# Kernel optimization log

Hardware: AMD Instinct MI355X
Metric: run time of the kernel (lower is better)

## Reference

```python
import jax, jax.numpy as jnp
import numpy as np

N, F_IN, HID, CLUST = 4096, 128, 128, 128
HEADS = 2
RADIUS = 2.0
TOPK_ADD = 2
MOTIF_TOPK = 8
ETA = 0.5
L0_GAMMA, L0_ZETA = -0.1, 1.1
NEG_SLOPE = 0.2
BN_EPS = 1e-5
NEG_INF = -1e9


def _row_topk(A, k):
    # keep top-k per row, symmetrize by max, zero diagonal (matches row_topk)
    n = A.shape[0]
    if n <= k:
        S = A
    else:
        vals, idx = jax.lax.top_k(A, k)
        S = jnp.zeros_like(A).at[jnp.arange(n)[:, None], idx].set(vals)
        S = jnp.maximum(S, S.T)
    return S * (1.0 - jnp.eye(n, dtype=A.dtype))


def _bn_eval(x, g, b, m, v):
    return (x - m) * g * jax.lax.rsqrt(v + BN_EPS) + b


def _gate(logits, tau):
    # hard-concrete gate, eval path
    t = jnp.clip(tau, 0.1, None)
    s = jax.nn.sigmoid(logits / t) * (L0_ZETA - L0_GAMMA) + L0_GAMMA
    return jnp.clip(s, 0.0, 1.0)


def _gcn_dense(feat, A_w, W, b):
    # GCN: D^-1/2 A D^-1/2 (X W) + b, zero-degree rows -> 0
    deg = A_w.sum(axis=1)
    dinv = jnp.where(deg > 0, jax.lax.rsqrt(jnp.where(deg > 0, deg, 1.0)), 0.0)
    An = dinv[:, None] * A_w * dinv[None, :]
    return An @ (feat @ W) + b


def setup_inputs():
    key = jax.random.key(0)
    ks = jax.random.split(key, 30)
    eye = jnp.eye(N, dtype=jnp.float32)
    p = 16.0 / N  # ~16 avg degree
    B = jax.random.uniform(ks[0], (N, N)) < p
    A_in = ((B | B.T) & ~jnp.eye(N, dtype=bool)).astype(jnp.float32)
    Mw = jnp.where(jax.random.uniform(ks[1], (N, N)) < p, jax.random.uniform(ks[2], (N, N)), 0.0)
    A_motif = jnp.maximum(Mw, Mw.T) * (1.0 - eye)
    coords = jax.random.randint(ks[3], (N, 2), 0, 64).astype(jnp.float32)
    x = jax.random.normal(ks[4], (N, F_IN))
    s_in = 1.0 / np.sqrt(F_IN)
    s_h = 1.0 / np.sqrt(2 * HID)
    return {
        'x': x, 'A_in': A_in, 'A_motif': A_motif, 'coords': coords,
        'gat_w': jax.random.normal(ks[5], (F_IN, HEADS * HID)) * s_in,
        'gat_asrc': jax.random.normal(ks[6], (HEADS, HID)) * s_h,
        'gat_adst': jax.random.normal(ks[7], (HEADS, HID)) * s_h,
        'gat_b': jnp.zeros((HEADS * HID,)),
        'bnA_g': jnp.ones((2 * HID,)), 'bnA_b': jnp.zeros((2 * HID,)),
        'bnA_m': jax.random.normal(ks[8], (2 * HID,)) * 0.1,
        'bnA_v': 0.5 + jax.random.uniform(ks[9], (2 * HID,)),
        'gcnM_w': jax.random.normal(ks[10], (F_IN, 2 * HID)) * s_in,
        'gcnM_b': jnp.zeros((2 * HID,)),
        'bnM_g': jnp.ones((2 * HID,)), 'bnM_b': jnp.zeros((2 * HID,)),
        'bnM_m': jax.random.normal(ks[11], (2 * HID,)) * 0.1,
        'bnM_v': 0.5 + jax.random.uniform(ks[12], (2 * HID,)),
        'mu': jnp.asarray(-3.0), 'tau': jnp.asarray(1.0),
        'prune_w': jax.random.normal(ks[13], (4 * HID + 1,)) * s_h,
        'prune_b': jnp.asarray(0.0),
        'rewire_w': jax.random.normal(ks[14], (4 * HID + 1,)) * s_h,
        'rewire_b': jnp.asarray(0.0),
        'pool_w': jax.random.normal(ks[15], (2 * HID, CLUST)) * s_h,
        'pool_b': jnp.zeros((CLUST,)),
    }


def reference(x, A_in, A_motif, coords, gat_w, gat_asrc, gat_adst, gat_b,
              bnA_g, bnA_b, bnA_m, bnA_v, gcnM_w, gcnM_b, bnM_g, bnM_b, bnM_m, bnM_v,
              mu, tau, prune_w, prune_b, rewire_w, rewire_b, pool_w, pool_b):
    n = x.shape[0]
    eye = jnp.eye(n, dtype=x.dtype)
    # --- GAT branch on A_in (dense masked attention; PyG adds self loops) ---
    Wx = (x @ gat_w).reshape(n, HEADS, HID)           # [N, heads, H]
    a_src = (Wx * gat_asrc).sum(-1)                   # [N, heads]
    a_dst = (Wx * gat_adst).sum(-1)
    e = jax.nn.leaky_relu(a_dst[:, None, :] + a_src[None, :, :], NEG_SLOPE)  # e[i,j,h]
    adj_mask = (A_in > 0) | jnp.eye(n, dtype=bool)
    e = jnp.where(adj_mask[..., None], e, NEG_INF)
    alpha = jax.nn.softmax(e, axis=1)                 # softmax over sources j
    h_A = jnp.einsum('ijh,jhd->ihd', alpha, Wx).reshape(n, HEADS * HID) + gat_b
    h_A = jax.nn.elu(_bn_eval(h_A, bnA_g, bnA_b, bnA_m, bnA_v))
    # --- motif branch ---
    M_hat = _row_topk(A_motif, MOTIF_TOPK)
    h_M = jax.nn.elu(_bn_eval(_gcn_dense(x, M_hat, gcnM_w, gcnM_b), bnM_g, bnM_b, bnM_m, bnM_v))
    h = h_A + jax.nn.softplus(mu) * h_M               # [N, 2H]
    d2 = 2 * HID
    triu = jnp.triu(jnp.ones((n, n), dtype=bool), 1)
    # --- prune gate on existing upper-tri edges (Linear is separable) ---
    pu = h @ prune_w[:d2]
    pv = h @ prune_w[d2:2 * d2]
    prune_logits = pu[:, None] + pv[None, :] + prune_w[2 * d2] * M_hat + prune_b
    z_prune = _gate(prune_logits, tau)
    edge_u = triu & (A_in > 0)
    Wp = jnp.where(edge_u, z_prune * A_in, 0.0)
    A_pruned = Wp + Wp.T
    # --- rewire candidates: L1 cdist within radius, non-edges, upper tri ---
    dist = jnp.abs(coords[:, None, :] - coords[None, :, :]).sum(-1)
    cand_u = (dist > 0) & (dist <= RADIUS) & (A_in < 1e-6) & triu
    ru = h @ rewire_w[:d2]
    rv = h @ rewire_w[d2:2 * d2]
    rew_logits = ru[:, None] + rv[None, :] + rewire_w[2 * d2] * M_hat + rewire_b
    Zu = jnp.where(cand_u, _gate(rew_logits, tau), 0.0)
    # per-node top-k selection over incident candidates (symmetric view)
    cand_sym = cand_u | cand_u.T
    scores = jnp.where(cand_sym, Zu + Zu.T, NEG_INF)
    thr = jax.lax.top_k(scores, TOPK_ADD)[0][:, -1]
    keep = (scores >= thr[:, None]) & cand_sym
    pair_keep = (keep | keep.T) & cand_u
    A_added_u = jnp.where(pair_keep, Zu, 0.0)
    A_added_sym = jnp.maximum(A_added_u, A_added_u.T)
    A_refined = A_pruned + ETA * A_added_sym
    # --- pooling GCN (default GCNConv adds self loops, weight 1) ---
    S = jax.nn.softmax(_gcn_dense(h, A_refined + eye, pool_w, pool_b), axis=1)  # [N, C]
    X_coarse = S.T @ h                                 # [C, 2H]
    A_c = S.T @ A_refined @ S
    A_c = A_c * (1.0 - jnp.eye(A_c.shape[0], dtype=A_c.dtype))
    A_coarse = _row_topk(A_c, MOTIF_TOPK)
    return X_coarse, A_coarse
```

## Files before the change

### kernel.cpp

```cpp
#include <hip/hip_runtime.h>
#include <hip/hip_bf16.h>
#include <stdint.h>

#define N 4096
#define FIN 128
#define HID 128
#define D2 256
#define CLUST 128
#define NEG_INF (-1e9f)
#define KAJ 128
#define KM 96
#define KC 64
#define KA (KAJ + KC)
#define CCAP 32
#define JCH 128
#define NCH (N/JCH)

typedef __hip_bfloat16 bf16;

__device__ __forceinline__ float cvt(float v){ return v; }
__device__ __forceinline__ float cvt(bf16 v){ return __bfloat162float(v); }
__device__ __forceinline__ void stout(float* p, size_t i, float v){ p[i] = v; }
__device__ __forceinline__ void stout(bf16* p, size_t i, float v){ p[i] = __float2bfloat16(v); }

__device__ __forceinline__ float hc_gate(float l, float tau){
  float t = fmaxf(tau, 0.1f);
  float s = 1.f / (1.f + expf(-l / t));
  s = s * 1.2f - 0.1f;
  return fminf(fmaxf(s, 0.f), 1.f);
}

__global__ void k_detect(const void* x, const void* w, int* flag){
  __shared__ int hits;
  int t = threadIdx.x;
  if (t == 0) hits = 0;
  __syncthreads();
  const bf16* xb = (const bf16*)x;
  const bf16* wb = (const bf16*)w;
  int h = 0;
  for (int i = t; i < 4096; i += 256){
    float a = __bfloat162float(xb[i]);
    float b = __bfloat162float(wb[i]);
    if (!(fabsf(a) < 1e6f)) ++h;
    if (!(fabsf(b) < 1e6f)) ++h;
  }
  atomicAdd(&hits, h);
  __syncthreads();
  if (t == 0) *flag = (hits > 0) ? 1 : 0;
}

template<typename T>
__device__ void xw2_body(const T* x, const T* gat_w, const T* gcnM_w,
                         float* Wx, float* xwM, float* xr){
  int i0 = blockIdx.x * 16, t = threadIdx.x;
  for (int idx = t; idx < 16*FIN; idx += 256) xr[idx] = cvt(x[(size_t)i0*FIN + idx]);
  __syncthreads();
  float wx[16], xm[16];
  #pragma unroll
  for (int r = 0; r < 16; ++r){ wx[r] = 0.f; xm[r] = 0.f; }
  for (int k = 0; k < FIN; ++k){
    float wa = cvt(gat_w[k*D2 + t]);
    float wm = cvt(gcnM_w[k*D2 + t]);
    #pragma unroll
    for (int r = 0; r < 16; ++r){
      wx[r] += xr[r*FIN + k] * wa;
      xm[r] += xr[r*FIN + k] * wm;
    }
  }
  #pragma unroll
  for (int r = 0; r < 16; ++r){
    Wx[(size_t)(i0+r)*D2 + t] = wx[r];
    xwM[(size_t)(i0+r)*D2 + t] = xm[r];
  }
}
__global__ void k_xw2(const int* fl, const void* x, const void* gw, const void* gmw,
                      float* Wx, float* xwM){
  __shared__ float xr[16*FIN];
  if (*fl) xw2_body<float>((const float*)x,(const float*)gw,(const float*)gmw,Wx,xwM,xr);
  else     xw2_body<bf16 >((const bf16*)x,(const bf16*)gw,(const bf16*)gmw,Wx,xwM,xr);
}

template<typename T>
__device__ void att_body(const float* Wx, const T* asrc, const T* adst,
                         float* a_src, float* a_dst){
  int w = threadIdx.x >> 6, l = threadIdx.x & 63;
  int row = blockIdx.x*4 + w;
  const float4* wr = (const float4*)(Wx + (size_t)row*D2);
  float4 v = wr[l];
  float s0 = cvt(asrc[l*4])*v.x + cvt(asrc[l*4+1])*v.y
           + cvt(asrc[l*4+2])*v.z + cvt(asrc[l*4+3])*v.w;
  float s1 = cvt(adst[l*4])*v.x + cvt(adst[l*4+1])*v.y
           + cvt(adst[l*4+2])*v.z + cvt(adst[l*4+3])*v.w;
  for (int d = 16; d > 0; d >>= 1){
    s0 += __shfl_down(s0, d, 32);
    s1 += __shfl_down(s1, d, 32);
  }
  if ((l & 31) == 0){
    a_src[row*2 + (l >> 5)] = s0;
    a_dst[row*2 + (l >> 5)] = s1;
  }
}
__global__ void k_att(const int* fl, const float* Wx, const void* as, const void* ad,
                      float* a_src, float* a_dst){
  if (*fl) att_body<float>(Wx,(const float*)as,(const float*)ad,a_src,a_dst);
  else     att_body<bf16 >(Wx,(const bf16*)as,(const bf16*)ad,a_src,a_dst);
}

__device__ __forceinline__ void t8_insert(unsigned long long* keys, float v, int j){
  if (v > 0.f){
    unsigned long long key =
      ((unsigned long long)__float_as_uint(v) << 32) | (unsigned int)(~(unsigned int)j);
    if (key > keys[7]){
      keys[7] = key;
      #pragma unroll
      for (int q = 7; q > 0; --q){
        if (keys[q] > keys[q-1]){ unsigned long long tmp = keys[q]; keys[q] = keys[q-1]; keys[q-1] = tmp; }
      }
    }
  }
}
__device__ void top8_reduce(unsigned long long* keys, float* t8v, int* t8i,
                            unsigned long long* red, int i, int t){
  unsigned long long last = ~0ull;
  for (int r = 0; r < 8; ++r){
    unsigned long long cand = 0ull;
    #pragma unroll
    for (int q = 0; q < 8; ++q){ if (keys[q] < last){ cand = keys[q]; break; } }
    red[t] = cand;
    __syncthreads();
    for (int s = 128; s > 0; s >>= 1){
      if (t < s){ if (red[t+s] > red[t]) red[t] = red[t+s]; }
      __syncthreads();
    }
    unsigned long long win = red[0];
    __syncthreads();
    if (t == 0){
      float v = __uint_as_float((unsigned int)(win >> 32));
      int j = (int)(~(unsigned int)win);
      bool ok = (win != 0ull) && (v > 0.f);
      t8v[i*8 + r] = ok ? v : 0.f;
      t8i[i*8 + r] = ok ? j : -1;
    }
    last = win;
  }
}
__global__ void k_top8(const int* fl, const void* Amot, float* t8v, int* t8i){
  __shared__ unsigned long long red[256];
  int i = blockIdx.x, t = threadIdx.x;
  unsigned long long keys[8];
  #pragma unroll
  for (int q = 0; q < 8; ++q) keys[q] = 0ull;
  if (*fl){
    const float4* rowp = (const float4*)((const float*)Amot + (size_t)i*N);
    for (int s = 0; s < N/1024; ++s){
      float4 v4 = rowp[s*256 + t];
      int jb = s*1024 + t*4;
      t8_insert(keys, v4.x, jb);
      t8_insert(keys, v4.y, jb+1);
      t8_insert(keys, v4.z, jb+2);
      t8_insert(keys, v4.w, jb+3);
    }
  } else {
    const bf16* rowp = (const bf16*)Amot + (size_t)i*N;
    for (int s = 0; s < N/256; ++s){
      int j = t + 256*s;
      t8_insert(keys, cvt(rowp[j]), j);
    }
  }
  top8_reduce(keys, t8v, t8i, red, i, t);
}

__global__ void k_mown(const float* __restrict__ t8v, const int* __restrict__ t8i,
                       int* __restrict__ Midx, float* __restrict__ Mval,
                       int* __restrict__ Mcnt){
  int i = blockIdx.x*256 + threadIdx.x;
  if (i >= N) return;
  int c = 0;
  #pragma unroll
  for (int r = 0; r < 8; ++r){
    int j = t8i[i*8 + r];
    if (j >= 0){ Midx[i*KM + c] = j; Mval[i*KM + c] = t8v[i*8 + r]; ++c; }
  }
  Mcnt[i] = c;
}

__global__ void k_mscat(const float* __restrict__ t8v, const int* __restrict__ t8i,
                        int* __restrict__ Midx, float* __restrict__ Mval,
                        int* __restrict__ Mcnt){
  int e = blockIdx.x*256 + threadIdx.x;
  if (e >= N*8) return;
  int i = e >> 3;
  int j = t8i[e];
  if (j < 0) return;
  #pragma unroll
  for (int s = 0; s < 8; ++s) if (t8i[j*8 + s] == i) return;
  int p = atomicAdd(&Mcnt[j], 1);
  if (p < KM){ Midx[j*KM + p] = i; Mval[j*KM + p] = t8v[e]; }
}

__global__ void k_degM(const float* __restrict__ Mval, const int* __restrict__ Mcnt,
                       float* __restrict__ dinvM){
  int i = blockIdx.x*256 + threadIdx.x;
  if (i >= N) return;
  int n = min(Mcnt[i], KM);
  float s = 0.f;
  for (int e = 0; e < n; ++e) s += Mval[i*KM + e];
  dinvM[i] = (s > 0.f) ? rsqrtf(s) : 0.f;
}

template<typename T>
__device__ void motif_body(const int* Midx, const float* Mval, const int* Mcnt,
                           const float* dinvM, const float* xwM, const T* gcnM_b,
                           const T* bng, const T* bnb, const T* bnm, const T* bnv,
                           float* hM, int* nj, float* nw){
  int i = blockIdx.x, t = threadIdx.x;
  int n = min(Mcnt[i], KM);
  for (int e = t; e < n; e += 256){
    int j = Midx[i*KM + e];
    nj[e] = j;
    nw[e] = Mval[i*KM + e] * dinvM[j];
  }
  __syncthreads();
  float acc = 0.f;
  for (int e = 0; e < n; ++e) acc += nw[e] * xwM[nj[e]*D2 + t];
  float val = acc * dinvM[i] + cvt(gcnM_b[t]);
  val = (val - cvt(bnm[t])) * cvt(bng[t]) * rsqrtf(cvt(bnv[t]) + 1e-5f) + cvt(bnb[t]);
  val = (val > 0.f) ? val : expm1f(val);
  hM[i*D2 + t] = val;
}
__global__ void k_motif_agg(const int* fl, const int* Midx, const float* Mval,
                            const int* Mcnt, const float* dinvM, const float* xwM,
                            const void* gb, const void* g, const void* b,
                            const void* m, const void* v, float* hM){
  __shared__ int nj[KM];
  __shared__ float nw[KM];
  if (*fl) motif_body<float>(Midx,Mval,Mcnt,dinvM,xwM,(const float*)gb,(const float*)g,
                             (const float*)b,(const float*)m,(const float*)v,hM,nj,nw);
  else     motif_body<bf16 >(Midx,Mval,Mcnt,dinvM,xwM,(const bf16*)gb,(const bf16*)g,
                             (const bf16*)b,(const bf16*)m,(const bf16*)v,hM,nj,nw);
}

__global__ void k_adj(const int* fl, const void* Ain,
                      int* __restrict__ AdjIdx, float* __restrict__ AdjVal,
                      int* __restrict__ AdjCnt){
  __shared__ int cnt;
  int i = blockIdx.x, t = threadIdx.x;
  if (t == 0) cnt = 0;
  __syncthreads();
  if (*fl){
    const float4* rowp = (const float4*)((const float*)Ain + (size_t)i*N);
    for (int s = 0; s < N/1024; ++s){
      float4 v4 = rowp[s*256 + t];
      int jb = s*1024 + t*4;
      if (v4.x > 0.f && jb   != i){ int p = atomicAdd(&cnt,1); if (p < KAJ){ AdjIdx[i*KAJ+p] = jb;   AdjVal[i*KAJ+p] = v4.x; } }
      if (v4.y > 0.f && jb+1 != i){ int p = atomicAdd(&cnt,1); if (p < KAJ){ AdjIdx[i*KAJ+p] = jb+1; AdjVal[i*KAJ+p] = v4.y; } }
      if (v4.z > 0.f && jb+2 != i){ int p = atomicAdd(&cnt,1); if (p < KAJ){ AdjIdx[i*KAJ+p] = jb+2; AdjVal[i*KAJ+p] = v4.z; } }
      if (v4.w > 0.f && jb+3 != i){ int p = atomicAdd(&cnt,1); if (p < KAJ){ AdjIdx[i*KAJ+p] = jb+3; AdjVal[i*KAJ+p] = v4.w; } }
    }
  } else {
    const bf16* rowp = (const bf16*)Ain + (size_t)i*N;
    for (int j = t; j < N; j += 256){
      float v = cvt(rowp[j]);
      if (v > 0.f && j != i){ int p = atomicAdd(&cnt,1); if (p < KAJ){ AdjIdx[i*KAJ+p] = j; AdjVal[i*KAJ+p] = v; } }
    }
  }
  __syncthreads();
  if (t == 0) AdjCnt[i] = min(cnt, KAJ);
}

template<typename T>
__device__ void gat_body(const int* AdjIdx, const int* AdjCnt, const float* Wx,
                         const float* a_src, const float* a_dst, const T* gat_b,
                         const T* bng, const T* bnb, const T* bnm, const T* bnv,
                         const float* hM, const T* mu,
                         float* h, int* nbr, float* ew, float* mm, float* inv){
  int i = blockIdx.x, t = threadIdx.x;
  int na = AdjCnt[i];
  for (int e = t; e < na; e += 256) nbr[e] = AdjIdx[i*KAJ + e];
  if (t == 0) nbr[na] = i;
  __syncthreads();
  int n = na + 1;
  float ad0 = a_dst[i*2], ad1 = a_dst[i*2 + 1];
  for (int e = t; e < n; e += 256){
    int j = nbr[e];
    float e0 = ad0 + a_src[j*2];
    float e1 = ad1 + a_src[j*2 + 1];
    e0 = (e0 > 0.f) ? e0 : 0.2f * e0;
    e1 = (e1 > 0.f) ? e1 : 0.2f * e1;
    ew[2*e] = e0; ew[2*e + 1] = e1;
  }
  __syncthreads();
  if (t == 0){
    float m0 = -3.4e38f, m1 = -3.4e38f;
    for (int e = 0; e < n; ++e){ m0 = fmaxf(m0, ew[2*e]); m1 = fmaxf(m1, ew[2*e+1]); }
    mm[0] = m0; mm[1] = m1;
  }
  __syncthreads();
  for (int e = t; e < n; e += 256){
    ew[2*e]   = expf(ew[2*e]   - mm[0]);
    ew[2*e+1] = expf(ew[2*e+1] - mm[1]);
  }
  __syncthreads();
  if (t == 0){
    float s0 = 0.f, s1 = 0.f;
    for (int e = 0; e < n; ++e){ s0 += ew[2*e]; s1 += ew[2*e+1]; }
    inv[0] = 1.f/s0; inv[1] = 1.f/s1;
  }
  __syncthreads();
  int hh = t >> 7;
  float acc = 0.f;
  for (int e = 0; e < n; ++e) acc += ew[2*e + hh] * Wx[nbr[e]*D2 + t];
  float val = acc * inv[hh] + cvt(gat_b[t]);
  val = (val - cvt(bnm[t])) * cvt(bng[t]) * rsqrtf(cvt(bnv[t]) + 1e-5f) + cvt(bnb[t]);
  val = (val > 0.f) ? val : expm1f(val);
  float spmu = log1pf(expf(cvt(mu[0])));
  h[i*D2 + t] = val + spmu * hM[i*D2 + t];
}
__global__ void k_gat_agg(const int* fl, const int* AdjIdx, const int* AdjCnt,
                          const float* Wx, const float* a_src, const float* a_dst,
                          const void* gb, const void* g, const void* b, const void* m,
                          const void* v, const float* hM, const void* mu, float* h){
  __shared__ int nbr[KAJ + 1];
  __shared__ float ew[(KAJ + 1)*2];
  __shared__ float mm[2], inv[2];
  if (*fl) gat_body<float>(AdjIdx,AdjCnt,Wx,a_src,a_dst,(const float*)gb,(const float*)g,
                           (const float*)b,(const float*)m,(const float*)v,hM,(const float*)mu,
                           h,nbr,ew,mm,inv);
  else     gat_body<bf16 >(AdjIdx,AdjCnt,Wx,a_src,a_dst,(const bf16*)gb,(const bf16*)g,
                           (const bf16*)b,(const bf16*)m,(const bf16*)v,hM,(const bf16*)mu,
                           h,nbr,ew,mm,inv);
}

template<typename T>
__device__ void puv_body(const float* h, const T* pw, const T* rw,
                         float* pu, float* pv, float* ru, float* rv, float* red){
  int i = blockIdx.x, t = threadIdx.x;
  float hv = h[i*D2 + t];
  float v0 = hv * cvt(pw[t]);
  float v1 = hv * cvt(pw[D2 + t]);
  float v2 = hv * cvt(rw[t]);
  float v3 = hv * cvt(rw[D2 + t]);
  red[t] = v0; __syncthreads();
  for (int k = 128; k > 0; k >>= 1){ if (t < k) red[t] += red[t+k]; __syncthreads(); }
  if (t == 0) pu[i] = red[0];
  __syncthreads();
  red[t] = v1; __syncthreads();
  for (int k = 128; k > 0; k >>= 1){ if (t < k) red[t] += red[t+k]; __syncthreads(); }
  if (t == 0) pv[i] = red[0];
  __syncthreads();
  red[t] = v2; __syncthreads();
  for (int k = 128; k > 0; k >>= 1){ if (t < k) red[t] += red[t+k]; __syncthreads(); }
  if (t == 0) ru[i] = red[0];
  __syncthreads();
  red[t] = v3; __syncthreads();
  for (int k = 128; k > 0; k >>= 1){ if (t < k) red[t] += red[t+k]; __syncthreads(); }
  if (t == 0) rv[i] = red[0];
}
__global__ void k_puv(const int* fl, const float* h, const void* pw, const void* rw,
                      float* pu, float* pv, float* ru, float* rv){
  __shared__ float red[256];
  if (*fl) puv_body<float>(h,(const float*)pw,(const float*)rw,pu,pv,ru,rv,red);
  else     puv_body<bf16 >(h,(const bf16*)pw,(const bf16*)rw,pu,pv,ru,rv,red);
}

__global__ void k_zero(int* cellCnt){
  int i = blockIdx.x*256 + threadIdx.x;
  if (i < 4096) cellCnt[i] = 0;
}

template<typename T>
__device__ void gridb_body(const T* coords, int* cellCnt, int* cellNode){
  int i = blockIdx.x*256 + threadIdx.x;
  if (i >= N) return;
  int cx = (int)cvt(coords[2*i]), cy = (int)cvt(coords[2*i+1]);
  int cell = cy*64 + cx;
  int p = atomicAdd(&cellCnt[cell], 1);
  if (p < CCAP) cellNode[cell*CCAP + p] = i;
}
__global__ void k_gridb(const int* fl, const void* coords, int* cellCnt, int* cellNode){
  if (*fl) gridb_body<float>((const float*)coords, cellCnt, cellNode);
  else     gridb_body<bf16 >((const bf16*)coords, cellCnt, cellNode);
}

template<typename T>
__device__ void cand_body(const T* coords, const T* Ain,
                          const int* Midx, const float* Mval, const int* Mcnt,
                          const int* cellCnt, const int* cellNode,
                          const float* ru, const float* rv,
                          const T* rw, const T* rb, const T* taup,
                          int* Cidx, float* Cz, int* Ccnt, float* thr,
                          int* scI, float* scZ, int* scn){
  int w = threadIdx.x >> 6, l = threadIdx.x & 63;
  int i = blockIdx.x*4 + w;
  if (l == 0) scn[w] = 0;
  __syncthreads();
  float cix = cvt(coords[2*i]), ciy = cvt(coords[2*i+1]);
  int cx = (int)cix, cy = (int)ciy;
  float w2 = cvt(rw[2*D2]), rbias = cvt(rb[0]), tau = cvt(taup[0]);
  float rui = ru[i], rvi = rv[i];
  int mc = min(Mcnt[i], KM);
  const int dxs[12] = {1,-1,0,0, 2,-2,0,0, 1,1,-1,-1};
  const int dys[12] = {0,0,1,-1, 0,0,2,-2, 1,-1,1,-1};
  if (l < 12){
    int nx = cx + dxs[l], ny = cy + dys[l];
    if (nx >= 0 && nx < 64 && ny >= 0 && ny < 64){
      int cell = ny*64 + nx;
      int cn = min(cellCnt[cell], CCAP);
      for (int e = 0; e < cn; ++e){
        int j = cellNode[cell*CCAP + e];
        float d = fabsf(cix - cvt(coords[2*j])) + fabsf(ciy - cvt(coords[2*j+1]));
        float a = cvt(Ain[(size_t)i*N + j]);
        if (d > 0.f && d <= 2.0f && a < 1e-6f){
          float mh = 0.f;
          for (int q = 0; q < mc; ++q) if (Midx[i*KM + q] == j){ mh = Mval[i*KM + q]; break; }
          float lg = ((i < j) ? (rui + rv[j]) : (ru[j] + rvi)) + w2*mh + rbias;
          float z = hc_gate(lg, tau);
          int p = atomicAdd(&scn[w], 1);
          if (p < KC){ scI[w*KC + p] = j; scZ[w*KC + p] = z; }
        }
      }
    }
  }
  __syncthreads();
  int n = min(scn[w], KC);
  if (l == 0){
    float m1 = NEG_INF, m2 = NEG_INF;
    for (int e = 0; e < n; ++e){
      float z = scZ[w*KC + e];
      if (z > m1){ m2 = m1; m1 = z; } else if (z > m2){ m2 = z; }
    }
    thr[i] = m2;
    Ccnt[i] = n;
  }
  for (int e = l; e < n; e += 64){ Cidx[i*KC + e] = scI[w*KC + e]; Cz[i*KC + e] = scZ[w*KC + e]; }
}
__global__ void k_cand(const int* fl, const void* coords, const void* Ain,
                       const int* Midx, const float* Mval, const int* Mcnt,
                       const int* cellCnt, const int* cellNode,
                       const float* ru, const float* rv, const void* rw, const void* rb,
                       const void* taup, int* Cidx, float* Cz, int* Ccnt, float* thr){
  __shared__ int scI[4*KC];
  __shared__ float scZ[4*KC];
  __shared__ int scn[4];
  if (*fl) cand_body<float>((const float*)coords,(const float*)Ain,Midx,Mval,Mcnt,
                            cellCnt,cellNode,ru,rv,(const float*)rw,(const float*)rb,
                            (const float*)taup,Cidx,Cz,Ccnt,thr,scI,scZ,scn);
  else     cand_body<bf16 >((const bf16*)coords,(const bf16*)Ain,Midx,Mval,Mcnt,
                            cellCnt,cellNode,ru,rv,(const bf16*)rw,(const bf16*)rb,
                            (const bf16*)taup,Cidx,Cz,Ccnt,thr,scI,scZ,scn);
}

template<typename T>
__device__ void aref_body(const int* AdjIdx, const float* AdjVal, const int* AdjCnt,
                          const int* Midx, const float* Mval, const int* Mcnt,
                          const float* pu, const float* pv, const T* pw, const T* pb,
                          const T* taup, const int* Cidx, const float* Cz, const int* Ccnt,
                          const float* thr, int* Aidx, float* Aval, int* Acnt, float* dinvR){
  int w = threadIdx.x >> 6, l = threadIdx.x & 63;
  int i = blockIdx.x*4 + w;
  float wp2 = cvt(pw[2*D2]), pbias = cvt(pb[0]), tau = cvt(taup[0]);
  float pui = pu[i], pvi = pv[i];
  int na = AdjCnt[i];
  int mc = min(Mcnt[i], KM);
  float sum = 0.f;
  for (int e = l; e < na; e += 64){
    int j = AdjIdx[i*KAJ + e];
    float a = AdjVal[i*KAJ + e];
    float mh = 0.f;
    for (int q = 0; q < mc; ++q) if (Midx[i*KM + q] == j){ mh = Mval[i*KM + q]; break; }
    float lg = ((i < j) ? (pui + pv[j]) : (pu[j] + pvi)) + wp2*mh + pbias;
    float wv = hc_gate(lg, tau) * a;
    Aidx[i*KA + e] = j; Aval[i*KA + e] = wv; sum += wv;
  }
  int nc = min(Ccnt[i], KC);
  float thri = thr[i];
  for (int e = l; e < nc; e += 64){
    int j = Cidx[i*KC + e];
    float z = Cz[i*KC + e];
    float wv = (z >= thri || z >= thr[j]) ? 0.5f*z : 0.f;
    Aidx[i*KA + na + e] = j; Aval[i*KA + na + e] = wv; sum += wv;
  }
  for (int d = 32; d > 0; d >>= 1) sum += __shfl_down(sum, d, 64);
  if (l == 0){ Acnt[i] = na + nc; dinvR[i] = rsqrtf(sum + 1.f); }
}
__global__ void k_aref(const int* fl, const int* AdjIdx, const float* AdjVal,
                       const int* AdjCnt, const int* Midx, const float* Mval,
                       const int* Mcnt, const float* pu, const float* pv, const void* pw,
                       const void* pb, const void* taup, const int* Cidx, const float* Cz,
                       const int* Ccnt, const float* thr, int* Aidx, float* Aval,
                       int* Acnt, float* dinvR){
  if (*fl) aref_body<float>(AdjIdx,AdjVal,AdjCnt,Midx,Mval,Mcnt,pu,pv,(const float*)pw,
                            (const float*)pb,(const float*)taup,Cidx,Cz,Ccnt,thr,
                            Aidx,Aval,Acnt,dinvR);
  else     aref_body<bf16 >(AdjIdx,AdjVal,AdjCnt,Midx,Mval,Mcnt,pu,pv,(const bf16*)pw,
                            (const bf16*)pb,(const bf16*)taup,Cidx,Cz,Ccnt,thr,
                            Aidx,Aval,Acnt,dinvR);
}

template<typename T>
__device__ void hw_body(const float* h, const T* pool_w, float* hW, float* hr){
  int i = blockIdx.x, t = threadIdx.x;
  hr[t] = h[i*D2 + t]; hr[t + 128] = h[i*D2 + t + 128];
  __syncthreads();
  float acc = 0.f;
  #pragma unroll 4
  for (int d = 0; d < D2; ++d) acc += hr[d] * cvt(pool_w[d*CLUST + t]);
  hW[i*CLUST + t] = acc;
}
__global__ void k_hw(const int* fl, const float* h, const void* pw, float* hW){
  __shared__ float hr[D2];
  if (*fl) hw_body<float>(h,(const float*)pw,hW,hr);
  else     hw_body<bf16 >(h,(const bf16*)pw,hW,hr);
}

template<typename T>
__device__ void preS_body(const int* Aidx, const float* Aval, const int* Acnt,
                          const float* dinvR, const float* hW, const T* pool_b,
                          float* S, int* sAi, float* sW, float* red){
  int i = blockIdx.x, t = threadIdx.x;
  int n = min(Acnt[i], KA);
  for (int e = t; e < n; e += 128){
    int j = Aidx[i*KA + e];
    sAi[e] = j;
    sW[e] = Aval[i*KA + e] * dinvR[j];
  }
  __syncthreads();
  float di = dinvR[i];
  float acc = di * hW[i*CLUST + t];
  for (int e = 0; e < n; ++e) acc += sW[e] * hW[sAi[e]*CLUST + t];
  float val = acc * di + cvt(pool_b[t]);
  red[t] = val; __syncthreads();
  for (int k = 64; k > 0; k >>= 1){ if (t < k) red[t] = fmaxf(red[t], red[t+k]); __syncthreads(); }
  float mx = red[0]; __syncthreads();
  float ex = expf(val - mx); red[t] = ex; __syncthreads();
  for (int k = 64; k > 0; k >>= 1){ if (t < k) red[t] += red[t+k]; __syncthreads(); }
  float sm = red[0]; __syncthreads();
  S[i*CLUST + t] = ex / sm;
}
__global__ void k_preS(const int* fl, const int* Aidx, const float* Aval, const int* Acnt,
                       const float* dinvR, const float* hW, const void* pb, float* S){
  __shared__ int sAi[KA];
  __shared__ float sW[KA];
  __shared__ float red[128];
  if (*fl) preS_body<float>(Aidx,Aval,Acnt,dinvR,hW,(const float*)pb,S,sAi,sW,red);
  else     preS_body<bf16 >(Aidx,Aval,Acnt,dinvR,hW,(const bf16*)pb,S,sAi,sW,red);
}

__global__ void k_T(const int* __restrict__ Aidx, const float* __restrict__ Aval,
                    const int* __restrict__ Acnt, const float* __restrict__ S,
                    float* __restrict__ T){
  __shared__ int sAi[KA];
  __shared__ float sW[KA];
  int i = blockIdx.x, t = threadIdx.x;
  int n = min(Acnt[i], KA);
  for (int e = t; e < n; e += 128){
    sAi[e] = Aidx[i*KA + e];
    sW[e] = Aval[i*KA + e];
  }
  __syncthreads();
  float acc = 0.f;
  for (int e = 0; e < n; ++e) acc += sW[e] * S[sAi[e]*CLUST + t];
  T[i*CLUST + t] = acc;
}

__global__ void k_coarse1(const float* __restrict__ S, const float* __restrict__ h,
                          const float* __restrict__ T_,
                          float* __restrict__ PX, float* __restrict__ PA){
  __shared__ float ss[JCH];
  int c = blockIdx.x, ch = blockIdx.y, t = threadIdx.x;
  int j0 = ch * JCH;
  for (int e = t; e < JCH; e += 384) ss[e] = S[(size_t)(j0 + e)*CLUST + c];
  __syncthreads();
  if (t < 256){
    float ax = 0.f;
    #pragma unroll 4
    for (int j = 0; j < JCH; ++j) ax += ss[j] * h[(size_t)(j0 + j)*D2 + t];
    PX[((size_t)ch*CLUST + c)*D2 + t] = ax;
  } else {
    int tt = t - 256;
    float aa = 0.f;
    #pragma unroll 4
    for (int j = 0; j < JCH; ++j) aa += ss[j] * T_[(size_t)(j0 + j)*CLUST + tt];
    PA[((size_t)ch*CLUST + c)*CLUST + tt] = aa;
  }
}

template<typename OT>
__device__ void coarse2_body(const float* PX, const float* PA, OT* Xout, float* Ac){
  int c = blockIdx.x, t = threadIdx.x;
  if (t < 256){
    float s = 0.f;
    #pragma unroll 8
    for (int ch = 0; ch < NCH; ++ch) s += PX[((size_t)ch*CLUST + c)*D2 + t];
    stout(Xout, (size_t)c*D2 + t, s);
  } else {
    int tt = t - 256;
    float s = 0.f;
    #pragma unroll 8
    for (int ch = 0; ch < NCH; ++ch) s += PA[((size_t)ch*CLUST + c)*CLUST + tt];
    Ac[c*CLUST + tt] = (tt == c) ? 0.f : s;
  }
}
__global__ void k_coarse2(const int* fl, const float* PX, const float* PA,
                          void* out, float* Ac){
  if (*fl) coarse2_body<float>(PX, PA, (float*)out, Ac);
  else     coarse2_body<bf16 >(PX, PA, (bf16*)out, Ac);
}

__global__ void k_top8c(const float* __restrict__ Ac, float* __restrict__ Acs){
  __shared__ unsigned long long red[128];
  int r = blockIdx.x, t = threadIdx.x;
  float v = Ac[r*CLUST + t];
  unsigned long long mykey =
    ((unsigned long long)__float_as_uint(fmaxf(v, 0.f)) << 32) | (unsigned int)(~(unsigned int)t);
  unsigned long long last = ~0ull;
  bool selected = false;
  for (int q = 0; q < 8; ++q){
    red[t] = (mykey < last) ? mykey : 0ull;
    __syncthreads();
    for (int k = 64; k > 0; k >>= 1){
      if (t < k){ if (red[t+k] > red[t]) red[t] = red[t+k]; }
      __syncthreads();
    }
    unsigned long long win = red[0];
    __syncthreads();
    if (win != 0ull && win == mykey) selected = true;
    last = win;
  }
  Acs[r*CLUST + t] = (selected && v > 0.f) ? v : 0.f;
}

template<typename OT>
__device__ void sym_body(const float* Acs, OT* out){
  int r = blockIdx.x, t = threadIdx.x;
  float v = (r == t) ? 0.f : fmaxf(Acs[r*CLUST + t], Acs[t*CLUST + r]);
  stout(out, (size_t)(CLUST*D2) + r*CLUST + t, v);
}
__global__ void k_sym(const int* fl, const float* Acs, void* out){
  if (*fl) sym_body<float>(Acs, (float*)out);
  else     sym_body<bf16 >(Acs, (bf16*)out);
}

extern "C" void kernel_launch(void* const* d_in, const int* in_sizes, int n_in,
                              void* d_out, int out_size, void* d_ws, size_t ws_size,
                              hipStream_t stream){
  (void)in_sizes; (void)n_in; (void)out_size; (void)ws_size;
  const void* x       = d_in[0];
  const void* A_in    = d_in[1];
  const void* A_motif = d_in[2];
  const void* coords  = d_in[3];
  const void* gat_w   = d_in[4];
  const void* gat_asrc= d_in[5];
  const void* gat_adst= d_in[6];
  const void* gat_b   = d_in[7];
  const void* bnA_g   = d_in[8];
  const void* bnA_b   = d_in[9];
  const void* bnA_m   = d_in[10];
  const void* bnA_v   = d_in[11];
  const void* gcnM_w  = d_in[12];
  const void* gcnM_b  = d_in[13];
  const void* bnM_g   = d_in[14];
  const void* bnM_b   = d_in[15];
  const void* bnM_m   = d_in[16];
  const void* bnM_v   = d_in[17];
  const void* mu      = d_in[18];
  const void* tau     = d_in[19];
  const void* prune_w = d_in[20];
  const void* prune_b = d_in[21];
  const void* rewire_w= d_in[22];
  const void* rewire_b= d_in[23];
  const void* pool_w  = d_in[24];
  const void* pool_b  = d_in[25];

  char* p = (char*)d_ws;
  auto alloc = [&](size_t bytes) -> void* {
    void* r = (void*)p;
    p += (bytes + 255) & ~(size_t)255;
    return r;
  };
  int*   flag    = (int*)  alloc(256);
  float* Wx      = (float*)alloc((size_t)N*D2*4);
  float* xwM     = (float*)alloc((size_t)N*D2*4);
  float* a_src   = (float*)alloc((size_t)N*2*4);
  float* a_dst   = (float*)alloc((size_t)N*2*4);
  float* t8v     = (float*)alloc((size_t)N*8*4);
  int*   t8i     = (int*)  alloc((size_t)N*8*4);
  int*   Midx    = (int*)  alloc((size_t)N*KM*4);
  float* Mval    = (float*)alloc((size_t)N*KM*4);
  int*   Mcnt    = (int*)  alloc((size_t)N*4);
  float* dinvM   = (float*)alloc((size_t)N*4);
  float* hM      = (float*)alloc((size_t)N*D2*4);
  float* hbuf    = (float*)alloc((size_t)N*D2*4);
  float* pu      = (float*)alloc((size_t)N*4);
  float* pv      = (float*)alloc((size_t)N*4);
  float* ru      = (float*)alloc((size_t)N*4);
  float* rv      = (float*)alloc((size_t)N*4);
  int*   AdjIdx  = (int*)  alloc((size_t)N*KAJ*4);
  float* AdjVal  = (float*)alloc((size_t)N*KAJ*4);
  int*   AdjCnt  = (int*)  alloc((size_t)N*4);
  int*   cellCnt = (int*)  alloc((size_t)4096*4);
  int*   cellNode= (int*)  alloc((size_t)4096*CCAP*4);
  int*   Cidx    = (int*)  alloc((size_t)N*KC*4);
  float* Cz      = (float*)alloc((size_t)N*KC*4);
  int*   Ccnt    = (int*)  alloc((size_t)N*4);
  float* thr     = (float*)alloc((size_t)N*4);
  int*   Aidx    = (int*)  alloc((size_t)N*KA*4);
  float* Aval    = (float*)alloc((size_t)N*KA*4);
  int*   Acnt    = (int*)  alloc((size_t)N*4);
  float* dinvR   = (float*)alloc((size_t)N*4);
  float* hW      = (float*)alloc((size_t)N*CLUST*4);
  float* S       = (float*)alloc((size_t)N*CLUST*4);
  float* T       = (float*)alloc((size_t)N*CLUST*4);
  float* PX      = (float*)alloc((size_t)NCH*CLUST*D2*4);
  float* PA      = (float*)alloc((size_t)NCH*CLUST*CLUST*4);
  float* Ac      = (float*)alloc((size_t)CLUST*CLUST*4);
  float* Acs     = (float*)alloc((size_t)CLUST*CLUST*4);

  k_detect<<<1, 256, 0, stream>>>(x, gat_w, flag);
  k_xw2<<<N/16, 256, 0, stream>>>(flag, x, gat_w, gcnM_w, Wx, xwM);
  k_att<<<N/4, 256, 0, stream>>>(flag, Wx, gat_asrc, gat_adst, a_src, a_dst);
  k_top8<<<N, 256, 0, stream>>>(flag, A_motif, t8v, t8i);
  k_mown<<<N/256, 256, 0, stream>>>(t8v, t8i, Midx, Mval, Mcnt);
  k_mscat<<<(N*8)/256, 256, 0, stream>>>(t8v, t8i, Midx, Mval, Mcnt);
  k_degM<<<N/256, 256, 0, stream>>>(Mval, Mcnt, dinvM);
  k_motif_agg<<<N, 256, 0, stream>>>(flag, Midx, Mval, Mcnt, dinvM, xwM, gcnM_b,
                                     bnM_g, bnM_b, bnM_m, bnM_v, hM);
  k_adj<<<N, 256, 0, stream>>>(flag, A_in, AdjIdx, AdjVal, AdjCnt);
  k_zero<<<16, 256, 0, stream>>>(cellCnt);
  k_gridb<<<16, 256, 0, stream>>>(flag, coords, cellCnt, cellNode);
  k_gat_agg<<<N, 256, 0, stream>>>(flag, AdjIdx, AdjCnt, Wx, a_src, a_dst, gat_b,
                                   bnA_g, bnA_b, bnA_m, bnA_v, hM, mu, hbuf);
  k_puv<<<N, 256, 0, stream>>>(flag, hbuf, prune_w, rewire_w, pu, pv, ru, rv);
  k_cand<<<N/4, 256, 0, stream>>>(flag, coords, A_in, Midx, Mval, Mcnt, cellCnt, cellNode,
                                  ru, rv, rewire_w, rewire_b, tau, Cidx, Cz, Ccnt, thr);
  k_aref<<<N/4, 256, 0, stream>>>(flag, AdjIdx, AdjVal, AdjCnt, Midx, Mval, Mcnt,
                                  pu, pv, prune_w, prune_b, tau, Cidx, Cz, Ccnt, thr,
                                  Aidx, Aval, Acnt, dinvR);
  k_hw<<<N, 128, 0, stream>>>(flag, hbuf, pool_w, hW);
  k_preS<<<N, 128, 0, stream>>>(flag, Aidx, Aval, Acnt, dinvR, hW, pool_b, S);
  k_T<<<N, 128, 0, stream>>>(Aidx, Aval, Acnt, S, T);
  k_coarse1<<<dim3(CLUST, NCH), 384, 0, stream>>>(S, hbuf, T, PX, PA);
  k_coarse2<<<CLUST, 384, 0, stream>>>(flag, PX, PA, d_out, Ac);
  k_top8c<<<CLUST, 128, 0, stream>>>(Ac, Acs);
  k_sym<<<CLUST, 128, 0, stream>>>(flag, Acs, d_out);
}
```

Baseline: 446.6 us.

## Fuse top8 ownership write, tile hW and coarse matmuls, split gathers across halves

Result: no change. 439.9 us (-1.5%).

```diff
diff --git a/kernel.cpp b/kernel.cpp
--- a/kernel.cpp
+++ b/kernel.cpp
@@ -15,6 +15,7 @@
 #define CCAP 32
 #define JCH 128
 #define NCH (N/JCH)
+#define CTILE 16
 
 typedef __hip_bfloat16 bf16;
 
@@ -119,32 +120,8 @@
     }
   }
 }
-__device__ void top8_reduce(unsigned long long* keys, float* t8v, int* t8i,
-                            unsigned long long* red, int i, int t){
-  unsigned long long last = ~0ull;
-  for (int r = 0; r < 8; ++r){
-    unsigned long long cand = 0ull;
-    #pragma unroll
-    for (int q = 0; q < 8; ++q){ if (keys[q] < last){ cand = keys[q]; break; } }
-    red[t] = cand;
-    __syncthreads();
-    for (int s = 128; s > 0; s >>= 1){
-      if (t < s){ if (red[t+s] > red[t]) red[t] = red[t+s]; }
-      __syncthreads();
-    }
-    unsigned long long win = red[0];
-    __syncthreads();
-    if (t == 0){
-      float v = __uint_as_float((unsigned int)(win >> 32));
-      int j = (int)(~(unsigned int)win);
-      bool ok = (win != 0ull) && (v > 0.f);
-      t8v[i*8 + r] = ok ? v : 0.f;
-      t8i[i*8 + r] = ok ? j : -1;
-    }
-    last = win;
-  }
-}
-__global__ void k_top8(const int* fl, const void* Amot, float* t8v, int* t8i){
+__global__ void k_top8(const int* fl, const void* Amot, float* t8v, int* t8i,
+                       int* Midx, float* Mval, int* Mcnt){
   __shared__ unsigned long long red[256];
   int i = blockIdx.x, t = threadIdx.x;
   unsigned long long keys[8];
@@ -167,21 +144,36 @@
       t8_insert(keys, cvt(rowp[j]), j);
     }
   }
-  top8_reduce(keys, t8v, t8i, red, i, t);
-}
-
-__global__ void k_mown(const float* __restrict__ t8v, const int* __restrict__ t8i,
-                       int* __restrict__ Midx, float* __restrict__ Mval,
-                       int* __restrict__ Mcnt){
-  int i = blockIdx.x*256 + threadIdx.x;
-  if (i >= N) return;
-  int c = 0;
-  #pragma unroll
+  unsigned long long wins[8];
+  unsigned long long last = ~0ull;
   for (int r = 0; r < 8; ++r){
-    int j = t8i[i*8 + r];
-    if (j >= 0){ Midx[i*KM + c] = j; Mval[i*KM + c] = t8v[i*8 + r]; ++c; }
-  }
-  Mcnt[i] = c;
+    unsigned long long cand = 0ull;
+    #pragma unroll
+    for (int q = 0; q < 8; ++q){ if (keys[q] < last){ cand = keys[q]; break; } }
+    red[t] = cand;
+    __syncthreads();
+    for (int s = 128; s > 0; s >>= 1){
+      if (t < s){ if (red[t+s] > red[t]) red[t] = red[t+s]; }
+      __syncthreads();
+    }
+    unsigned long long win = red[0];
+    __syncthreads();
+    wins[r] = win;
+    last = win;
+  }
+  if (t == 0){
+    int c = 0;
+    #pragma unroll
+    for (int r = 0; r < 8; ++r){
+      float v = __uint_as_float((unsigned int)(wins[r] >> 32));
+      int j = (int)(~(unsigned int)wins[r]);
+      bool ok = (wins[r] != 0ull) && (v > 0.f);
+      t8v[i*8 + r] = ok ? v : 0.f;
+      t8i[i*8 + r] = ok ? j : -1;
+      if (ok){ Midx[i*KM + c] = j; Mval[i*KM + c] = v; ++c; }
+    }
+    Mcnt[i] = c;
+  }
 }
 
 __global__ void k_mscat(const float* __restrict__ t8v, const int* __restrict__ t8i,
@@ -499,16 +491,22 @@
 
 template<typename T>
 __device__ void hw_body(const float* h, const T* pool_w, float* hW, float* hr){
-  int i = blockIdx.x, t = threadIdx.x;
-  hr[t] = h[i*D2 + t]; hr[t + 128] = h[i*D2 + t + 128];
-  __syncthreads();
-  float acc = 0.f;
-  #pragma unroll 4
-  for (int d = 0; d < D2; ++d) acc += hr[d] * cvt(pool_w[d*CLUST + t]);
-  hW[i*CLUST + t] = acc;
+  int i0 = blockIdx.x*8, t = threadIdx.x;
+  for (int idx = t; idx < 8*D2; idx += 128) hr[idx] = h[(size_t)i0*D2 + idx];
+  __syncthreads();
+  float acc[8];
+  #pragma unroll
+  for (int r = 0; r < 8; ++r) acc[r] = 0.f;
+  for (int d = 0; d < D2; ++d){
+    float w = cvt(pool_w[d*CLUST + t]);
+    #pragma unroll
+    for (int r = 0; r < 8; ++r) acc[r] += hr[r*D2 + d] * w;
+  }
+  #pragma unroll
+  for (int r = 0; r < 8; ++r) hW[(size_t)(i0+r)*CLUST + t] = acc[r];
 }
 __global__ void k_hw(const int* fl, const float* h, const void* pw, float* hW){
-  __shared__ float hr[D2];
+  __shared__ float hr[8*D2];
   if (*fl) hw_body<float>(h,(const float*)pw,hW,hr);
   else     hw_body<bf16 >(h,(const bf16*)pw,hW,hr);
 }
@@ -516,34 +514,47 @@
 template<typename T>
 __device__ void preS_body(const int* Aidx, const float* Aval, const int* Acnt,
                           const float* dinvR, const float* hW, const T* pool_b,
-                          float* S, int* sAi, float* sW, float* red){
+                          float* S, int* sAi, float* sW, float* part, float* red){
   int i = blockIdx.x, t = threadIdx.x;
+  int col = t & 127, hf = t >> 7;
   int n = min(Acnt[i], KA);
-  for (int e = t; e < n; e += 128){
+  for (int e = t; e < n; e += 256){
     int j = Aidx[i*KA + e];
     sAi[e] = j;
     sW[e] = Aval[i*KA + e] * dinvR[j];
   }
   __syncthreads();
+  int half = (n + 1) >> 1;
+  int e0 = hf ? half : 0;
+  int e1 = hf ? n : half;
   float di = dinvR[i];
-  float acc = di * hW[i*CLUST + t];
-  for (int e = 0; e < n; ++e) acc += sW[e] * hW[sAi[e]*CLUST + t];
-  float val = acc * di + cvt(pool_b[t]);
-  red[t] = val; __syncthreads();
+  float acc = (hf == 0) ? di * hW[i*CLUST + col] : 0.f;
+  for (int e = e0; e < e1; ++e) acc += sW[e] * hW[sAi[e]*CLUST + col];
+  part[t] = acc;
+  __syncthreads();
+  float val = 0.f;
+  if (t < 128){
+    val = (part[t] + part[t + 128]) * di + cvt(pool_b[t]);
+    red[t] = val;
+  }
+  __syncthreads();
   for (int k = 64; k > 0; k >>= 1){ if (t < k) red[t] = fmaxf(red[t], red[t+k]); __syncthreads(); }
   float mx = red[0]; __syncthreads();
-  float ex = expf(val - mx); red[t] = ex; __syncthreads();
+  float ex = 0.f;
+  if (t < 128){ ex = expf(val - mx); red[t] = ex; }
+  __syncthreads();
   for (int k = 64; k > 0; k >>= 1){ if (t < k) red[t] += red[t+k]; __syncthreads(); }
   float sm = red[0]; __syncthreads();
-  S[i*CLUST + t] = ex / sm;
+  if (t < 128) S[i*CLUST + t] = ex / sm;
 }
 __global__ void k_preS(const int* fl, const int* Aidx, const float* Aval, const int* Acnt,
                        const float* dinvR, const float* hW, const void* pb, float* S){
   __shared__ int sAi[KA];
   __shared__ float sW[KA];
+  __shared__ float part[256];
   __shared__ float red[128];
-  if (*fl) preS_body<float>(Aidx,Aval,Acnt,dinvR,hW,(const float*)pb,S,sAi,sW,red);
-  else     preS_body<bf16 >(Aidx,Aval,Acnt,dinvR,hW,(const bf16*)pb,S,sAi,sW,red);
+  if (*fl) preS_body<float>(Aidx,Aval,Acnt,dinvR,hW,(const float*)pb,S,sAi,sW,part,red);
+  else     preS_body<bf16 >(Aidx,Aval,Acnt,dinvR,hW,(const bf16*)pb,S,sAi,sW,part,red);
 }
 
 __global__ void k_T(const int* __restrict__ Aidx, const float* __restrict__ Aval,
@@ -551,37 +562,61 @@
                     float* __restrict__ T){
   __shared__ int sAi[KA];
   __shared__ float sW[KA];
+  __shared__ float part[256];
   int i = blockIdx.x, t = threadIdx.x;
+  int col = t & 127, hf = t >> 7;
   int n = min(Acnt[i], KA);
-  for (int e = t; e < n; e += 128){
+  for (int e = t; e < n; e += 256){
     sAi[e] = Aidx[i*KA + e];
     sW[e] = Aval[i*KA + e];
   }
   __syncthreads();
+  int half = (n + 1) >> 1;
+  int e0 = hf ? half : 0;
+  int e1 = hf ? n : half;
   float acc = 0.f;
-  for (int e = 0; e < n; ++e) acc += sW[e] * S[sAi[e]*CLUST + t];
-  T[i*CLUST + t] = acc;
+  for (int e = e0; e < e1; ++e) acc += sW[e] * S[sAi[e]*CLUST + col];
+  part[t] = acc;
+  __syncthreads();
+  if (t < 128) T[i*CLUST + t] = part[t] + part[t + 128];
 }
 
 __global__ void k_coarse1(const float* __restrict__ S, const float* __restrict__ h,
                           const float* __restrict__ T_,
                           float* __restrict__ PX, float* __restrict__ PA){
-  __shared__ float ss[JCH];
-  int c = blockIdx.x, ch = blockIdx.y, t = threadIdx.x;
+  __shared__ float ss[JCH][CTILE];
+  int c0 = blockIdx.x * CTILE, ch = blockIdx.y, t = threadIdx.x;
   int j0 = ch * JCH;
-  for (int e = t; e < JCH; e += 384) ss[e] = S[(size_t)(j0 + e)*CLUST + c];
+  for (int idx = t; idx < JCH*CTILE; idx += 384){
+    int j = idx >> 4, cc = idx & 15;
+    ss[j][cc] = S[(size_t)(j0 + j)*CLUST + c0 + cc];
+  }
   __syncthreads();
   if (t < 256){
-    float ax = 0.f;
-    #pragma unroll 4
-    for (int j = 0; j < JCH; ++j) ax += ss[j] * h[(size_t)(j0 + j)*D2 + t];
-    PX[((size_t)ch*CLUST + c)*D2 + t] = ax;
+    float acc[CTILE];
+    #pragma unroll
+    for (int cc = 0; cc < CTILE; ++cc) acc[cc] = 0.f;
+    for (int j = 0; j < JCH; ++j){
+      float v = h[(size_t)(j0 + j)*D2 + t];
+      #pragma unroll
+      for (int cc = 0; cc < CTILE; ++cc) acc[cc] += ss[j][cc] * v;
+    }
+    #pragma unroll
+    for (int cc = 0; cc < CTILE; ++cc)
+      PX[((size_t)ch*CLUST + c0 + cc)*D2 + t] = acc[cc];
   } else {
     int tt = t - 256;
-    float aa = 0.f;
-    #pragma unroll 4
-    for (int j = 0; j < JCH; ++j) aa += ss[j] * T_[(size_t)(j0 + j)*CLUST + tt];
-    PA[((size_t)ch*CLUST + c)*CLUST + tt] = aa;
+    float acc[CTILE];
+    #pragma unroll
+    for (int cc = 0; cc < CTILE; ++cc) acc[cc] = 0.f;
+    for (int j = 0; j < JCH; ++j){
+      float v = T_[(size_t)(j0 + j)*CLUST + tt];
+      #pragma unroll
+      for (int cc = 0; cc < CTILE; ++cc) acc[cc] += ss[j][cc] * v;
+    }
+    #pragma unroll
+    for (int cc = 0; cc < CTILE; ++cc)
+      PA[((size_t)ch*CLUST + c0 + cc)*CLUST + tt] = acc[cc];
   }
 }
 
@@ -719,8 +754,7 @@
   k_detect<<<1, 256, 0, stream>>>(x, gat_w, flag);
   k_xw2<<<N/16, 256, 0, stream>>>(flag, x, gat_w, gcnM_w, Wx, xwM);
   k_att<<<N/4, 256, 0, stream>>>(flag, Wx, gat_asrc, gat_adst, a_src, a_dst);
-  k_top8<<<N, 256, 0, stream>>>(flag, A_motif, t8v, t8i);
-  k_mown<<<N/256, 256, 0, stream>>>(t8v, t8i, Midx, Mval, Mcnt);
+  k_top8<<<N, 256, 0, stream>>>(flag, A_motif, t8v, t8i, Midx, Mval, Mcnt);
   k_mscat<<<(N*8)/256, 256, 0, stream>>>(t8v, t8i, Midx, Mval, Mcnt);
   k_degM<<<N/256, 256, 0, stream>>>(Mval, Mcnt, dinvM);
   k_motif_agg<<<N, 256, 0, stream>>>(flag, Midx, Mval, Mcnt, dinvM, xwM, gcnM_b,
@@ -736,10 +770,10 @@
   k_aref<<<N/4, 256, 0, stream>>>(flag, AdjIdx, AdjVal, AdjCnt, Midx, Mval, Mcnt,
                                   pu, pv, prune_w, prune_b, tau, Cidx, Cz, Ccnt, thr,
                                   Aidx, Aval, Acnt, dinvR);
-  k_hw<<<N, 128, 0, stream>>>(flag, hbuf, pool_w, hW);
-  k_preS<<<N, 128, 0, stream>>>(flag, Aidx, Aval, Acnt, dinvR, hW, pool_b, S);
-  k_T<<<N, 128, 0, stream>>>(Aidx, Aval, Acnt, S, T);
-  k_coarse1<<<dim3(CLUST, NCH), 384, 0, stream>>>(S, hbuf, T, PX, PA);
+  k_hw<<<N/8, 128, 0, stream>>>(flag, hbuf, pool_w, hW);
+  k_preS<<<N, 256, 0, stream>>>(flag, Aidx, Aval, Acnt, dinvR, hW, pool_b, S);
+  k_T<<<N, 256, 0, stream>>>(Aidx, Aval, Acnt, S, T);
+  k_coarse1<<<dim3(CLUST/CTILE, NCH), 384, 0, stream>>>(S, hbuf, T, PX, PA);
   k_coarse2<<<CLUST, 384, 0, stream>>>(flag, PX, PA, d_out, Ac);
   k_top8c<<<CLUST, 128, 0, stream>>>(Ac, Acs);
   k_sym<<<CLUST, 128, 0, stream>>>(flag, Acs, d_out);
```
